# Performance work log

Hardware: AMD Instinct MI355X
Metric: run time of the kernel (lower is better)

## Reference

```python
import jax, jax.numpy as jnp
import numpy as np

N_EXPERTS = 16
NUM_SHARDS = 1
CAPACITY_FACTOR = 1.25
EPS = 0.01


def setup_inputs() -> dict:
    key = jax.random.key(0)
    k1, k2, k3 = jax.random.split(key, 3)
    C, T, D = 4, 4096, 1024
    E = N_EXPERTS * NUM_SHARDS
    inputs = jax.random.normal(k1, (C, T, D), dtype=jnp.float32)
    # trunc-normal router weight, std = (initializer_factor / ((D + E)/2))**0.5
    std = (1.0 / ((D + E) / 2.0)) ** 0.5
    router_weight = jax.random.truncated_normal(k2, -2.0, 2.0, (E, D), dtype=jnp.float32) * std
    # multiplicative jitter in [1-eps, 1+eps)
    noise = (1.0 - EPS) + 2.0 * EPS * jax.random.uniform(k3, (C, T, D), dtype=jnp.float32)
    return {"inputs": inputs, "router_weight": router_weight, "noise": noise}


def reference(inputs, router_weight, noise):
    C, T, D = inputs.shape
    E = N_EXPERTS * NUM_SHARDS
    expert_capacity = max(int(CAPACITY_FACTOR * T // N_EXPERTS), 1)

    x = inputs.astype(jnp.float32) * noise                      # gate inputs with jitter
    router_logits = jnp.einsum('ctd,ed->cte', x, router_weight)  # [C,T,E]
    router_probs = jax.nn.softmax(router_logits, axis=-1)
    expert_gate = jnp.max(router_probs, axis=-1)                 # [C,T]
    expert_index = jnp.argmax(router_probs, axis=-1)             # [C,T] int

    expert_mask = jax.nn.one_hot(expert_index, E, dtype=jnp.float32)  # [C,T,E]

    # load-balancing aux loss (before capacity truncation)
    density1 = expert_mask.mean(axis=1)          # [C,E]
    density1_proxy = router_probs.mean(axis=1)   # [C,E]
    aux_loss = (density1 * density1_proxy).sum() * E

    # capacity-limited position tracking
    position_in_expert = jnp.cumsum(expert_mask, axis=1) * expert_mask            # [C,T,E]
    expert_mask = expert_mask * (position_in_expert.astype(jnp.int32) < expert_capacity)
    expert_mask_flat = expert_mask.sum(axis=-1)                                    # [C,T]
    position_in_expert = (jnp.cumsum(expert_mask, axis=1) * expert_mask).astype(jnp.int32)
    expert_gate = expert_gate * expert_mask_flat

    # Faithful replication of torch scatter_(dim=1) on a [C,T,E,1] tensor with
    # index shape [C,T,1,1]: only the (e=0, cap=0) slice is written, at token
    # position == expert_index[c,t].
    c_idx = jnp.arange(C)[:, None]
    expert_index_inf = jnp.zeros((C, T, E, 1), jnp.float32).at[c_idx, expert_index, 0, 0].set(1.0)

    # one-hot over capacity slot (scatter along dim 3)
    position_inf = jax.nn.one_hot(position_in_expert, expert_capacity, dtype=jnp.float32)  # [C,T,E,cap]

    combine_tensor = (expert_gate[:, :, None, None]
                      * expert_mask_flat[:, :, None, None]
                      * expert_index_inf
                      * position_inf)
    dispatch_tensor = combine_tensor.astype(bool)
    return dispatch_tensor, combine_tensor, aux_loss
```

## Files before the change

### kernel.cpp

```cpp
#include <hip/hip_runtime.h>
#include <math.h>

#define C_DIM 4
#define T_DIM 4096
#define D_DIM 1024
#define E_DIM 16
#define CAP   320
#define CT    (C_DIM * T_DIM)
#define OUT_ONE ((size_t)CT * E_DIM * CAP)

#define NBLOCKS 1024
#define N4      ((2 * OUT_ONE) / 4)
#define F4_PER_BLOCK (N4 / NBLOCKS)

__host__ __device__ constexpr int bitrev6(int i) {
    return ((i & 1) << 5) | ((i & 2) << 3) | ((i & 4) << 1)
         | ((i & 8) >> 1) | ((i & 16) >> 3) | ((i & 32) >> 5);
}


__device__ __forceinline__ void do_router(
    const float* __restrict__ in, const float* __restrict__ w,
    const float* __restrict__ noise, float* __restrict__ gate,
    int* __restrict__ index, float* __restrict__ auxpart,
    int* __restrict__ counts, float* psum, int* hcnt)
{
    const int tid = threadIdx.x;
    if (tid < E_DIM) { psum[tid] = 0.0f; hcnt[tid] = 0; }
    __syncthreads();

    const int wave = tid >> 6;
    const int lane = tid & 63;
    const int g0   = blockIdx.x * 16 + wave * 4;

    float val[64];
    #pragma unroll
    for (int i = 0; i < 64; ++i) val[i] = 0.0f;

    #pragma unroll
    for (int r = 0; r < 4; ++r) {
        const int d0 = r * 256 + lane * 4;
        float4 x[4];
        #pragma unroll
        for (int tk = 0; tk < 4; ++tk) {
            const float4 a = *(const float4*)(in    + (size_t)(g0 + tk) * D_DIM + d0);
            const float4 n = *(const float4*)(noise + (size_t)(g0 + tk) * D_DIM + d0);
            x[tk] = make_float4(a.x * n.x, a.y * n.y, a.z * n.z, a.w * n.w);
        }
        #pragma unroll
        for (int e = 0; e < 16; ++e) {
            const float4 wv = *(const float4*)(w + e * D_DIM + d0);
            #pragma unroll
            for (int tk = 0; tk < 4; ++tk) {
                val[bitrev6(tk * 16 + e)] += x[tk].x * wv.x + x[tk].y * wv.y
                                           + x[tk].z * wv.z + x[tk].w * wv.w;
            }
        }
    }

    #pragma unroll
    for (int m = 0; m < 6; ++m) {
        const int half = 32 >> m;
        const int bit  = (lane >> m) & 1;
        #pragma unroll
        for (int j = 0; j < half; ++j) {
            const float send = bit ? val[j] : val[j + half];
            const float recv = __shfl_xor(send, 1 << m, 64);
            val[j] = (bit ? val[j + half] : val[j]) + recv;
        }
    }

    const int tk = lane >> 4;
    const int e  = lane & 15;
    const float logit = val[0];
    const int g = g0 + tk;

    float mv = logit; int am = e;
    #pragma unroll
    for (int msk = 1; msk <= 8; msk <<= 1) {
        const float ov = __shfl_xor(mv, msk, 64);
        const int   oe = __shfl_xor(am, msk, 64);
        if (ov > mv || (ov == mv && oe < am)) { mv = ov; am = oe; }
    }

    const float p = __expf(logit - mv);
    float s = p;
    #pragma unroll
    for (int msk = 1; msk <= 8; msk <<= 1)
        s += __shfl_xor(s, msk, 64);

    const float inv = 1.0f / s;
    if (e == am) {
        gate[g]  = inv;
        index[g] = am;
        atomicAdd(&hcnt[am], 1);
    }

    float pn = p * inv;
    pn += __shfl_xor(pn, 16, 64);
    pn += __shfl_xor(pn, 32, 64);
    if (lane < 16)
        atomicAdd(&psum[e], pn);

    __syncthreads();
    if (tid < 16) {
        const int c = blockIdx.x >> 8;
        atomicAdd(&auxpart[c * 16 + tid], psum[tid]);
        atomicAdd(&counts [c * 16 + tid], hcnt[tid]);
    }
}

__device__ __forceinline__ void do_fill(float4* __restrict__ out4)
{
    const float4 z = make_float4(0.f, 0.f, 0.f, 0.f);
    float4* dst = out4 + (size_t)blockIdx.x * F4_PER_BLOCK;
    #pragma unroll 4
    for (int i = threadIdx.x; i < F4_PER_BLOCK; i += 256)
        dst[i] = z;
}

__global__ __launch_bounds__(256) void fused_router_fill_kernel(
    const float* __restrict__ in, const float* __restrict__ w,
    const float* __restrict__ noise, float* __restrict__ gate,
    int* __restrict__ index, float* __restrict__ auxpart,
    int* __restrict__ counts, float4* __restrict__ out4)
{
    __shared__ float psum[E_DIM];
    __shared__ int   hcnt[E_DIM];

    if (blockIdx.x & 1) {
        do_fill(out4);
        do_router(in, w, noise, gate, index, auxpart, counts, psum, hcnt);
    } else {
        do_router(in, w, noise, gate, index, auxpart, counts, psum, hcnt);
        do_fill(out4);
    }
}

__global__ __launch_bounds__(64) void finalize_kernel(
    const float* __restrict__ gate, const int* __restrict__ index,
    const int* __restrict__ counts, const float* __restrict__ auxpart,
    float* __restrict__ out)
{
    const int id = threadIdx.x;
    const int c  = id >> 4;
    const int tp = id & 15;
    const int cnt = counts[id];

    float term = ((float)cnt * (1.0f / T_DIM)) * (auxpart[id] * (1.0f / T_DIM));

    if (cnt > 0) {
        const int g     = c * T_DIM + tp;
        const int myidx = index[g];
        int s = 0;
        if (myidx == 0) {
            int r = 0;
            for (int t = 0; t <= tp; ++t)
                r += (index[c * T_DIM + t] == 0);
            s = r;
        }
        const size_t off = ((size_t)g * E_DIM + 0) * CAP + (size_t)s;
        out[off]            = 1.0f;
        out[OUT_ONE + off]  = gate[g];
    }

    #pragma unroll
    for (int off = 32; off; off >>= 1)
        term += __shfl_down(term, off, 64);
    if (id == 0)
        out[2 * OUT_ONE] = 16.0f * term;
}

extern "C" void kernel_launch(void* const* d_in, const int* in_sizes, int n_in,
                              void* d_out, int out_size, void* d_ws, size_t ws_size,
                              hipStream_t stream) {
    const float* in    = (const float*)d_in[0];
    const float* w     = (const float*)d_in[1];
    const float* noise = (const float*)d_in[2];
    float* out = (float*)d_out;

    char* ws = (char*)d_ws;
    float* auxpart = (float*)(ws);
    int*   counts  = (int*)(ws + 256);
    float* gate    = (float*)(ws + 512);
    int*   index   = (int*)(ws + 512 + 65536);

    (void)hipMemsetAsync(ws, 0, 512, stream);

    fused_router_fill_kernel<<<dim3(NBLOCKS), dim3(256), 0, stream>>>(
        in, w, noise, gate, index, auxpart, counts, (float4*)out);
    finalize_kernel<<<dim3(1), dim3(64), 0, stream>>>(gate, index, counts, auxpart, out);
}
```

Measured before the change: 170.8 us.

## Use one token per wave and quadruple block count in fused router/fill

Each wave now computes logits for a single token instead of four, cutting the accumulator array from 64 to 16 registers and shortening the butterfly reduction. The grid grows from 1024 to 4096 blocks, so each block zero-fills a quarter as much output and the router work is spread more finely. The shared-memory init and the global atomic flush move to the kernel body, and the fill loop unroll rises to 8. Weight reads are reused across fewer tokens per wave, and there are four times as many per-block global atomics.

```diff
diff --git a/kernel.cpp b/kernel.cpp
--- a/kernel.cpp
+++ b/kernel.cpp
@@ -9,58 +9,45 @@
 #define CT    (C_DIM * T_DIM)
 #define OUT_ONE ((size_t)CT * E_DIM * CAP)
 
-#define NBLOCKS 1024
+#define NBLOCKS 4096
 #define N4      ((2 * OUT_ONE) / 4)
 #define F4_PER_BLOCK (N4 / NBLOCKS)
 
-__host__ __device__ constexpr int bitrev6(int i) {
-    return ((i & 1) << 5) | ((i & 2) << 3) | ((i & 4) << 1)
-         | ((i & 8) >> 1) | ((i & 16) >> 3) | ((i & 32) >> 5);
+__host__ __device__ constexpr int bitrev4(int i) {
+    return ((i & 1) << 3) | ((i & 2) << 1) | ((i & 4) >> 1) | ((i & 8) >> 3);
 }
 
 
 __device__ __forceinline__ void do_router(
     const float* __restrict__ in, const float* __restrict__ w,
     const float* __restrict__ noise, float* __restrict__ gate,
-    int* __restrict__ index, float* __restrict__ auxpart,
-    int* __restrict__ counts, float* psum, int* hcnt)
+    int* __restrict__ index, float* psum, int* hcnt)
 {
-    const int tid = threadIdx.x;
-    if (tid < E_DIM) { psum[tid] = 0.0f; hcnt[tid] = 0; }
-    __syncthreads();
-
+    const int tid  = threadIdx.x;
     const int wave = tid >> 6;
     const int lane = tid & 63;
-    const int g0   = blockIdx.x * 16 + wave * 4;
+    const int g    = blockIdx.x * 4 + wave;
 
-    float val[64];
+    float val[16];
     #pragma unroll
-    for (int i = 0; i < 64; ++i) val[i] = 0.0f;
+    for (int i = 0; i < 16; ++i) val[i] = 0.0f;
 
     #pragma unroll
     for (int r = 0; r < 4; ++r) {
         const int d0 = r * 256 + lane * 4;
-        float4 x[4];
-        #pragma unroll
-        for (int tk = 0; tk < 4; ++tk) {
-            const float4 a = *(const float4*)(in    + (size_t)(g0 + tk) * D_DIM + d0);
-            const float4 n = *(const float4*)(noise + (size_t)(g0 + tk) * D_DIM + d0);
-            x[tk] = make_float4(a.x * n.x, a.y * n.y, a.z * n.z, a.w * n.w);
-        }
+        const float4 a = *(const float4*)(in    + (size_t)g * D_DIM + d0);
+        const float4 n = *(const float4*)(noise + (size_t)g * D_DIM + d0);
+        const float4 x = make_float4(a.x * n.x, a.y * n.y, a.z * n.z, a.w * n.w);
         #pragma unroll
         for (int e = 0; e < 16; ++e) {
             const float4 wv = *(const float4*)(w + e * D_DIM + d0);
-            #pragma unroll
-            for (int tk = 0; tk < 4; ++tk) {
-                val[bitrev6(tk * 16 + e)] += x[tk].x * wv.x + x[tk].y * wv.y
-                                           + x[tk].z * wv.z + x[tk].w * wv.w;
-            }
+            val[bitrev4(e)] += x.x * wv.x + x.y * wv.y + x.z * wv.z + x.w * wv.w;
         }
     }
 
     #pragma unroll
-    for (int m = 0; m < 6; ++m) {
-        const int half = 32 >> m;
+    for (int m = 0; m < 4; ++m) {
+        const int half = 8 >> m;
         const int bit  = (lane >> m) & 1;
         #pragma unroll
         for (int j = 0; j < half; ++j) {
@@ -69,11 +56,11 @@
             val[j] = (bit ? val[j + half] : val[j]) + recv;
         }
     }
+    float logit = val[0];
+    logit += __shfl_xor(logit, 16, 64);
+    logit += __shfl_xor(logit, 32, 64);
 
-    const int tk = lane >> 4;
-    const int e  = lane & 15;
-    const float logit = val[0];
-    const int g = g0 + tk;
+    const int e = lane & 15;
 
     float mv = logit; int am = e;
     #pragma unroll
@@ -90,31 +77,20 @@
         s += __shfl_xor(s, msk, 64);
 
     const float inv = 1.0f / s;
-    if (e == am) {
+    if (lane < 16 && e == am) {
         gate[g]  = inv;
         index[g] = am;
         atomicAdd(&hcnt[am], 1);
     }
-
-    float pn = p * inv;
-    pn += __shfl_xor(pn, 16, 64);
-    pn += __shfl_xor(pn, 32, 64);
     if (lane < 16)
-        atomicAdd(&psum[e], pn);
-
-    __syncthreads();
-    if (tid < 16) {
-        const int c = blockIdx.x >> 8;
-        atomicAdd(&auxpart[c * 16 + tid], psum[tid]);
-        atomicAdd(&counts [c * 16 + tid], hcnt[tid]);
-    }
+        atomicAdd(&psum[e], p * inv);
 }
 
 __device__ __forceinline__ void do_fill(float4* __restrict__ out4)
 {
     const float4 z = make_float4(0.f, 0.f, 0.f, 0.f);
     float4* dst = out4 + (size_t)blockIdx.x * F4_PER_BLOCK;
-    #pragma unroll 4
+    #pragma unroll 8
     for (int i = threadIdx.x; i < F4_PER_BLOCK; i += 256)
         dst[i] = z;
 }
@@ -127,13 +103,23 @@
 {
     __shared__ float psum[E_DIM];
     __shared__ int   hcnt[E_DIM];
+    const int tid = threadIdx.x;
+    if (tid < E_DIM) { psum[tid] = 0.0f; hcnt[tid] = 0; }
+    __syncthreads();
 
     if (blockIdx.x & 1) {
         do_fill(out4);
-        do_router(in, w, noise, gate, index, auxpart, counts, psum, hcnt);
+        do_router(in, w, noise, gate, index, psum, hcnt);
     } else {
-        do_router(in, w, noise, gate, index, auxpart, counts, psum, hcnt);
+        do_router(in, w, noise, gate, index, psum, hcnt);
         do_fill(out4);
+    }
+
+    __syncthreads();
+    if (tid < 16) {
+        const int c = blockIdx.x >> 10;
+        atomicAdd(&auxpart[c * 16 + tid], psum[tid]);
+        atomicAdd(&counts [c * 16 + tid], hcnt[tid]);
     }
 }
 
```

New measurement: 194.2 us. 1.14x slower.
